# Optimization experiments

Hardware: AMD Instinct MI355X
Metric: run time of the kernel (lower is better)

The kernel has to match this reference:

```python
import jax, jax.numpy as jnp
import numpy as np

L, B, NH, S, H, K, NC = 12, 16, 12, 128, 768, 16, 2
ALPHA, BETA = 0.1, 0.1


def setup_inputs() -> dict:
    key = jax.random.key(0)
    ks = jax.random.split(key, 10)
    voted_logit = jax.random.normal(ks[0], (B, NC), jnp.float32)
    target = jax.random.randint(ks[1], (B,), 0, NC)
    t_hid = jax.random.normal(ks[2], (L, B, S, H), jnp.float32)
    s_hid = jax.random.normal(ks[3], (L, B, S, H), jnp.float32)
    t_att = jax.random.normal(ks[4], (L, B, NH, S, S), jnp.float32)
    s_att = jax.random.normal(ks[5], (L, B, NH, S, S), jnp.float32)

    def make_align(k):
        k1, k2 = jax.random.split(k)
        starts = jax.random.randint(k1, (B, K), 0, S - 9)
        lens = jax.random.randint(k2, (B, K), 1, 9)
        return jnp.stack([starts, starts + lens], axis=-1).astype(jnp.int32)  # [B,K,2]

    t_align = make_align(ks[6])
    s_align = make_align(ks[7])
    cs_len = jax.random.randint(ks[8], (B,), 0, K + 1).astype(jnp.int32)
    return {
        "voted_logit": voted_logit, "target": target,
        "t_hidden_states": t_hid, "t_att_matrices": t_att,
        "s_hidden_states": s_hid, "s_att_matrices": s_att,
        "teacher_cs_token_align": t_align, "student_cs_token_align": s_align,
        "cs_token_align_len": cs_len,
    }


def _span_mean_hidden(h, aligns):
    # h: [L,B,S,H], aligns: [B,K,2] -> mean over each span: [L,B,K,H]
    c = jnp.pad(jnp.cumsum(h, axis=2), ((0, 0), (0, 0), (1, 0), (0, 0)))
    s, e = aligns[..., 0], aligns[..., 1]  # [B,K]
    seg = (jnp.take_along_axis(c, e[None, :, :, None], axis=2)
           - jnp.take_along_axis(c, s[None, :, :, None], axis=2))
    ln = jnp.maximum(e - s, 1).astype(h.dtype)
    return seg / ln[None, :, :, None]


def _span_mean_attn(a, aligns):
    # a: [L,B,NH,S,S], aligns: [B,K,2] -> mean over query-span: [L,B,NH,K,S]
    c = jnp.pad(jnp.cumsum(a, axis=3), ((0, 0), (0, 0), (0, 0), (1, 0), (0, 0)))
    s, e = aligns[..., 0], aligns[..., 1]  # [B,K]
    seg = (jnp.take_along_axis(c, e[None, :, None, :, None], axis=3)
           - jnp.take_along_axis(c, s[None, :, None, :, None], axis=3))
    ln = jnp.maximum(e - s, 1).astype(a.dtype)
    return seg / ln[None, :, None, :, None]


def reference(voted_logit, target, t_hidden_states, t_att_matrices,
              s_hidden_states, s_att_matrices, teacher_cs_token_align,
              student_cs_token_align, cs_token_align_len):
    # zero out masked (-inf style) attention entries
    t_att = jnp.where(t_att_matrices <= -100.0, 0.0, t_att_matrices)
    s_att = jnp.where(s_att_matrices <= -100.0, 0.0, s_att_matrices)

    mask = (jnp.arange(K)[None, :] < cs_token_align_len[:, None])  # [B,K] valid spans
    n_spans = mask.sum().astype(jnp.float32)
    maskf = mask.astype(jnp.float32)

    # hidden-state span means: [L,B,K,H]
    t_hm = _span_mean_hidden(t_hidden_states, teacher_cs_token_align)
    s_hm = _span_mean_hidden(s_hidden_states, student_cs_token_align)
    hid_sq = jnp.sum(((t_hm - s_hm) ** 2) * maskf[None, :, :, None])
    hid_denom = jnp.maximum(n_spans * L * H, 1.0)
    hidn_loss = jnp.where(n_spans > 0, ALPHA * hid_sq / hid_denom, 0.0)

    # attention span means: [L,B,NH,K,S]
    t_am = _span_mean_attn(t_att, teacher_cs_token_align)
    s_am = _span_mean_attn(s_att, student_cs_token_align)
    att_sq = jnp.sum(((t_am - s_am) ** 2) * maskf[None, :, None, :, None])
    att_denom = jnp.maximum(n_spans * L * NH * S, 1.0)
    attn_loss = jnp.where(n_spans > 0, BETA * att_sq / att_denom, 0.0)

    # cross-entropy
    logp = jax.nn.log_softmax(voted_logit, axis=-1)
    pred_loss = -jnp.take_along_axis(logp, target[:, None], axis=1).mean()

    return (hidn_loss, attn_loss, pred_loss)
```

## Files before the change

kernel.cpp:

```cpp
#include <hip/hip_runtime.h>

#define L_   12
#define B_   16
#define NH_  12
#define S_   128
#define H_   768
#define K_   16
#define NC_  2
#define ALPHA_ 0.1f
#define BETA_  0.1f

__device__ __forceinline__ float waveReduceSum(float v) {
#pragma unroll
    for (int off = 32; off > 0; off >>= 1)
        v += __shfl_down(v, off, 64);
    return v;
}

__global__ void __launch_bounds__(256)
hid_loss_kernel(const float* __restrict__ t_hid,
                const float* __restrict__ s_hid,
                const int* __restrict__ t_align,
                const int* __restrict__ s_align,
                const int* __restrict__ cs_len,
                float* __restrict__ acc) {
    int idx = blockIdx.x;
    int k = idx % K_;
    int b = (idx / K_) % B_;
    int l = idx / (K_ * B_);
    if (k >= cs_len[b]) return;

    int ts = t_align[(b * K_ + k) * 2 + 0];
    int te = t_align[(b * K_ + k) * 2 + 1];
    int ss = s_align[(b * K_ + k) * 2 + 0];
    int se = s_align[(b * K_ + k) * 2 + 1];
    float inv_lt = 1.0f / (float)max(te - ts, 1);
    float inv_ls = 1.0f / (float)max(se - ss, 1);

    const float* tb = t_hid + (size_t)(l * B_ + b) * S_ * H_;
    const float* sb = s_hid + (size_t)(l * B_ + b) * S_ * H_;
    int tid = threadIdx.x;

    float st0 = 0.f, st1 = 0.f, st2 = 0.f;
    for (int s = ts; s < te; ++s) {
        const float* r = tb + (size_t)s * H_;
        st0 += r[tid];
        st1 += r[tid + 256];
        st2 += r[tid + 512];
    }
    float su0 = 0.f, su1 = 0.f, su2 = 0.f;
    for (int s = ss; s < se; ++s) {
        const float* r = sb + (size_t)s * H_;
        su0 += r[tid];
        su1 += r[tid + 256];
        su2 += r[tid + 512];
    }
    float d0 = st0 * inv_lt - su0 * inv_ls;
    float d1 = st1 * inv_lt - su1 * inv_ls;
    float d2 = st2 * inv_lt - su2 * inv_ls;
    float sq = d0 * d0 + d1 * d1 + d2 * d2;

    sq = waveReduceSum(sq);
    __shared__ float wsum[4];
    int wid = tid >> 6, lane = tid & 63;
    if (lane == 0) wsum[wid] = sq;
    __syncthreads();
    if (tid == 0)
        atomicAdd(acc, wsum[0] + wsum[1] + wsum[2] + wsum[3]);
}

__global__ void __launch_bounds__(128)
att_loss_kernel(const float* __restrict__ t_att,
                const float* __restrict__ s_att,
                const int* __restrict__ t_align,
                const int* __restrict__ s_align,
                const int* __restrict__ cs_len,
                float* __restrict__ acc) {
    int idx = blockIdx.x;
    int k = idx % K_;
    int nh = (idx / K_) % NH_;
    int b = (idx / (K_ * NH_)) % B_;
    int l = idx / (K_ * NH_ * B_);
    if (k >= cs_len[b]) return;

    int ts = t_align[(b * K_ + k) * 2 + 0];
    int te = t_align[(b * K_ + k) * 2 + 1];
    int ss = s_align[(b * K_ + k) * 2 + 0];
    int se = s_align[(b * K_ + k) * 2 + 1];
    float inv_lt = 1.0f / (float)max(te - ts, 1);
    float inv_ls = 1.0f / (float)max(se - ss, 1);

    const float* tb = t_att + (((size_t)(l * B_ + b) * NH_ + nh)) * S_ * S_;
    const float* sb = s_att + (((size_t)(l * B_ + b) * NH_ + nh)) * S_ * S_;
    int tid = threadIdx.x;

    float at = 0.f;
    for (int q = ts; q < te; ++q) {
        float v = tb[(size_t)q * S_ + tid];
        at += (v <= -100.0f) ? 0.0f : v;
    }
    float as = 0.f;
    for (int q = ss; q < se; ++q) {
        float v = sb[(size_t)q * S_ + tid];
        as += (v <= -100.0f) ? 0.0f : v;
    }
    float d = at * inv_lt - as * inv_ls;
    float sq = d * d;

    sq = waveReduceSum(sq);
    __shared__ float wsum[2];
    int wid = tid >> 6, lane = tid & 63;
    if (lane == 0) wsum[wid] = sq;
    __syncthreads();
    if (tid == 0)
        atomicAdd(acc + 1, wsum[0] + wsum[1]);
}

__global__ void __launch_bounds__(64)
finalize_kernel(const float* __restrict__ acc,
                const float* __restrict__ voted,
                const int* __restrict__ target,
                const int* __restrict__ cs_len,
                float* __restrict__ out) {
    int lane = threadIdx.x;

    float ns = (lane < B_) ? (float)cs_len[lane] : 0.f;
    ns = waveReduceSum(ns);
    ns = __shfl(ns, 0, 64);

    float pl = 0.f;
    if (lane < B_) {
        float a = voted[lane * NC_ + 0];
        float b = voted[lane * NC_ + 1];
        float m = fmaxf(a, b);
        float lse = m + logf(expf(a - m) + expf(b - m));
        float lp = voted[lane * NC_ + target[lane]] - lse;
        pl = -lp;
    }
    pl = waveReduceSum(pl);

    if (lane == 0) {
        float hid = (ns > 0.f)
            ? ALPHA_ * acc[0] / fmaxf(ns * (float)L_ * (float)H_, 1.0f) : 0.f;
        float att = (ns > 0.f)
            ? BETA_ * acc[1] / fmaxf(ns * (float)L_ * (float)NH_ * (float)S_, 1.0f) : 0.f;
        out[0] = hid;
        out[1] = att;
        out[2] = pl / (float)B_;
    }
}

extern "C" void kernel_launch(void* const* d_in, const int* in_sizes, int n_in,
                              void* d_out, int out_size, void* d_ws, size_t ws_size,
                              hipStream_t stream) {
    const float* voted   = (const float*)d_in[0];
    const int*   target  = (const int*)d_in[1];
    const float* t_hid   = (const float*)d_in[2];
    const float* t_att   = (const float*)d_in[3];
    const float* s_hid   = (const float*)d_in[4];
    const float* s_att   = (const float*)d_in[5];
    const int*   t_align = (const int*)d_in[6];
    const int*   s_align = (const int*)d_in[7];
    const int*   cs_len  = (const int*)d_in[8];
    float* out = (float*)d_out;
    float* acc = (float*)d_ws;

    hipMemsetAsync(acc, 0, 2 * sizeof(float), stream);

    hid_loss_kernel<<<L_ * B_ * K_, 256, 0, stream>>>(
        t_hid, s_hid, t_align, s_align, cs_len, acc);

    att_loss_kernel<<<L_ * B_ * NH_ * K_, 128, 0, stream>>>(
        t_att, s_att, t_align, s_align, cs_len, acc);

    finalize_kernel<<<1, 64, 0, stream>>>(acc, voted, target, cs_len, out);
}
```

Baseline: 574.3 us.

## Fuse hidden and attention loss kernels with vectorized unrolled span loads

Result: no change. 568.3 us (-1.0%).

```diff
diff --git a/kernel.cpp b/kernel.cpp
--- a/kernel.cpp
+++ b/kernel.cpp
@@ -10,6 +10,9 @@
 #define ALPHA_ 0.1f
 #define BETA_  0.1f
 
+#define NB_HID (L_ * B_ * K_)
+#define NB_ATT (L_ * B_ * NH_ * K_)
+
 __device__ __forceinline__ float waveReduceSum(float v) {
 #pragma unroll
     for (int off = 32; off > 0; off >>= 1)
@@ -17,103 +20,110 @@
     return v;
 }
 
-__global__ void __launch_bounds__(256)
-hid_loss_kernel(const float* __restrict__ t_hid,
-                const float* __restrict__ s_hid,
-                const int* __restrict__ t_align,
-                const int* __restrict__ s_align,
-                const int* __restrict__ cs_len,
-                float* __restrict__ acc) {
-    int idx = blockIdx.x;
-    int k = idx % K_;
-    int b = (idx / K_) % B_;
-    int l = idx / (K_ * B_);
-    if (k >= cs_len[b]) return;
+__global__ void __launch_bounds__(64)
+fused_loss_kernel(const float* __restrict__ t_hid,
+                  const float* __restrict__ s_hid,
+                  const float* __restrict__ t_att,
+                  const float* __restrict__ s_att,
+                  const int* __restrict__ t_align,
+                  const int* __restrict__ s_align,
+                  const int* __restrict__ cs_len,
+                  float* __restrict__ acc) {
+    int bid = blockIdx.x;
+    int lane = threadIdx.x;
 
-    int ts = t_align[(b * K_ + k) * 2 + 0];
-    int te = t_align[(b * K_ + k) * 2 + 1];
-    int ss = s_align[(b * K_ + k) * 2 + 0];
-    int se = s_align[(b * K_ + k) * 2 + 1];
-    float inv_lt = 1.0f / (float)max(te - ts, 1);
-    float inv_ls = 1.0f / (float)max(se - ss, 1);
+    if (bid < NB_HID) {
+        int k = bid % K_;
+        int b = (bid / K_) % B_;
+        int l = bid / (K_ * B_);
+        if (k >= cs_len[b]) return;
 
-    const float* tb = t_hid + (size_t)(l * B_ + b) * S_ * H_;
-    const float* sb = s_hid + (size_t)(l * B_ + b) * S_ * H_;
-    int tid = threadIdx.x;
+        int2 tsp = ((const int2*)t_align)[b * K_ + k];
+        int2 ssp = ((const int2*)s_align)[b * K_ + k];
+        int ts = tsp.x, te = tsp.y, ss = ssp.x, se = ssp.y;
+        float inv_lt = 1.0f / (float)max(te - ts, 1);
+        float inv_ls = 1.0f / (float)max(se - ss, 1);
 
-    float st0 = 0.f, st1 = 0.f, st2 = 0.f;
-    for (int s = ts; s < te; ++s) {
-        const float* r = tb + (size_t)s * H_;
-        st0 += r[tid];
-        st1 += r[tid + 256];
-        st2 += r[tid + 512];
+        const float4* tb = (const float4*)t_hid + (size_t)(l * B_ + b) * (S_ * H_ / 4);
+        const float4* sb = (const float4*)s_hid + (size_t)(l * B_ + b) * (S_ * H_ / 4);
+
+        float sq = 0.f;
+#pragma unroll
+        for (int c = 0; c < 3; ++c) {
+            int col = lane + c * 64;
+            float4 tv[8], sv[8];
+#pragma unroll
+            for (int r = 0; r < 8; ++r)
+                tv[r] = tb[min(ts + r, te - 1) * (H_ / 4) + col];
+#pragma unroll
+            for (int r = 0; r < 8; ++r)
+                sv[r] = sb[min(ss + r, se - 1) * (H_ / 4) + col];
+
+            float4 st = make_float4(0.f, 0.f, 0.f, 0.f);
+            float4 su = make_float4(0.f, 0.f, 0.f, 0.f);
+#pragma unroll
+            for (int r = 0; r < 8; ++r) {
+                if (ts + r < te) {
+                    st.x += tv[r].x; st.y += tv[r].y;
+                    st.z += tv[r].z; st.w += tv[r].w;
+                }
+                if (ss + r < se) {
+                    su.x += sv[r].x; su.y += sv[r].y;
+                    su.z += sv[r].z; su.w += sv[r].w;
+                }
+            }
+            float dx = st.x * inv_lt - su.x * inv_ls;
+            float dy = st.y * inv_lt - su.y * inv_ls;
+            float dz = st.z * inv_lt - su.z * inv_ls;
+            float dw = st.w * inv_lt - su.w * inv_ls;
+            sq += dx * dx + dy * dy + dz * dz + dw * dw;
+        }
+        sq = waveReduceSum(sq);
+        if (lane == 0) atomicAdd(acc + 0, sq);
+    } else {
+        int idx = bid - NB_HID;
+        int k = idx % K_;
+        int nh = (idx / K_) % NH_;
+        int b = (idx / (K_ * NH_)) % B_;
+        int l = idx / (K_ * NH_ * B_);
+        if (k >= cs_len[b]) return;
+
+        int2 tsp = ((const int2*)t_align)[b * K_ + k];
+        int2 ssp = ((const int2*)s_align)[b * K_ + k];
+        int ts = tsp.x, te = tsp.y, ss = ssp.x, se = ssp.y;
+        float inv_lt = 1.0f / (float)max(te - ts, 1);
+        float inv_ls = 1.0f / (float)max(se - ss, 1);
+
+        const float2* tb = (const float2*)t_att
+            + (size_t)((l * B_ + b) * NH_ + nh) * (S_ * S_ / 2);
+        const float2* sb = (const float2*)s_att
+            + (size_t)((l * B_ + b) * NH_ + nh) * (S_ * S_ / 2);
+
+        float2 tv[8], sv[8];
+#pragma unroll
+        for (int r = 0; r < 8; ++r)
+            tv[r] = tb[min(ts + r, te - 1) * (S_ / 2) + lane];
+#pragma unroll
+        for (int r = 0; r < 8; ++r)
+            sv[r] = sb[min(ss + r, se - 1) * (S_ / 2) + lane];
+
+        float atx = 0.f, aty = 0.f, asx = 0.f, asy = 0.f;
+#pragma unroll
+        for (int r = 0; r < 8; ++r) {
+            if (ts + r < te) {
+                atx += (tv[r].x > -100.0f) ? tv[r].x : 0.f;
+                aty += (tv[r].y > -100.0f) ? tv[r].y : 0.f;
+            }
+            if (ss + r < se) {
+                asx += (sv[r].x > -100.0f) ? sv[r].x : 0.f;
+                asy += (sv[r].y > -100.0f) ? sv[r].y : 0.f;
+            }
+        }
+        float dx = atx * inv_lt - asx * inv_ls;
+        float dy = aty * inv_lt - asy * inv_ls;
+        float sq = waveReduceSum(dx * dx + dy * dy);
+        if (lane == 0) atomicAdd(acc + 1, sq);
     }
-    float su0 = 0.f, su1 = 0.f, su2 = 0.f;
-    for (int s = ss; s < se; ++s) {
-        const float* r = sb + (size_t)s * H_;
-        su0 += r[tid];
-        su1 += r[tid + 256];
-        su2 += r[tid + 512];
-    }
-    float d0 = st0 * inv_lt - su0 * inv_ls;
-    float d1 = st1 * inv_lt - su1 * inv_ls;
-    float d2 = st2 * inv_lt - su2 * inv_ls;
-    float sq = d0 * d0 + d1 * d1 + d2 * d2;
-
-    sq = waveReduceSum(sq);
-    __shared__ float wsum[4];
-    int wid = tid >> 6, lane = tid & 63;
-    if (lane == 0) wsum[wid] = sq;
-    __syncthreads();
-    if (tid == 0)
-        atomicAdd(acc, wsum[0] + wsum[1] + wsum[2] + wsum[3]);
-}
-
-__global__ void __launch_bounds__(128)
-att_loss_kernel(const float* __restrict__ t_att,
-                const float* __restrict__ s_att,
-                const int* __restrict__ t_align,
-                const int* __restrict__ s_align,
-                const int* __restrict__ cs_len,
-                float* __restrict__ acc) {
-    int idx = blockIdx.x;
-    int k = idx % K_;
-    int nh = (idx / K_) % NH_;
-    int b = (idx / (K_ * NH_)) % B_;
-    int l = idx / (K_ * NH_ * B_);
-    if (k >= cs_len[b]) return;
-
-    int ts = t_align[(b * K_ + k) * 2 + 0];
-    int te = t_align[(b * K_ + k) * 2 + 1];
-    int ss = s_align[(b * K_ + k) * 2 + 0];
-    int se = s_align[(b * K_ + k) * 2 + 1];
-    float inv_lt = 1.0f / (float)max(te - ts, 1);
-    float inv_ls = 1.0f / (float)max(se - ss, 1);
-
-    const float* tb = t_att + (((size_t)(l * B_ + b) * NH_ + nh)) * S_ * S_;
-    const float* sb = s_att + (((size_t)(l * B_ + b) * NH_ + nh)) * S_ * S_;
-    int tid = threadIdx.x;
-
-    float at = 0.f;
-    for (int q = ts; q < te; ++q) {
-        float v = tb[(size_t)q * S_ + tid];
-        at += (v <= -100.0f) ? 0.0f : v;
-    }
-    float as = 0.f;
-    for (int q = ss; q < se; ++q) {
-        float v = sb[(size_t)q * S_ + tid];
-        as += (v <= -100.0f) ? 0.0f : v;
-    }
-    float d = at * inv_lt - as * inv_ls;
-    float sq = d * d;
-
-    sq = waveReduceSum(sq);
-    __shared__ float wsum[2];
-    int wid = tid >> 6, lane = tid & 63;
-    if (lane == 0) wsum[wid] = sq;
-    __syncthreads();
-    if (tid == 0)
-        atomicAdd(acc + 1, wsum[0] + wsum[1]);
 }
 
 __global__ void __launch_bounds__(64)
@@ -167,11 +177,8 @@
 
     hipMemsetAsync(acc, 0, 2 * sizeof(float), stream);
 
-    hid_loss_kernel<<<L_ * B_ * K_, 256, 0, stream>>>(
-        t_hid, s_hid, t_align, s_align, cs_len, acc);
-
-    att_loss_kernel<<<L_ * B_ * NH_ * K_, 128, 0, stream>>>(
-        t_att, s_att, t_align, s_align, cs_len, acc);
+    fused_loss_kernel<<<NB_HID + NB_ATT, 64, 0, stream>>>(
+        t_hid, s_hid, t_att, s_att, t_align, s_align, cs_len, acc);
 
     finalize_kernel<<<1, 64, 0, stream>>>(acc, voted, target, cs_len, out);
 }
```
